# Optimization experiments

Measured on AMD Instinct MI355X. Metric: run time of the kernel, lower is better.

The kernel has to match this reference:

```python
import jax, jax.numpy as jnp
import numpy as np

DIM = 1024
HEADS = 16
HIDDEN = 2048  # dim * mlp_ratio
EPS = 1e-6


def _rmsnorm(x, scale):
    # faithful to torch: x * (scale / (norm / (sqrt(d) + eps)))
    norm = jnp.linalg.norm(x, axis=-1, keepdims=True)
    return x * (scale * (x.shape[-1] ** 0.5 + EPS) / norm)


def setup_inputs() -> dict:
    key = jax.random.key(0)
    ks = jax.random.split(key, 8)
    B, N, C = 4, 4096, DIM
    s = 0.02
    return {
        "x": jax.random.normal(ks[0], (B, N, C), dtype=jnp.float32),
        "scale1": jnp.ones((C,), jnp.float32),
        "scale2": jnp.ones((C,), jnp.float32),
        "gamma": jnp.ones((C,), jnp.float32),
        "qkv_w": jax.random.normal(ks[1], (3 * C, C), jnp.float32) * s,
        "proj_w": jax.random.normal(ks[2], (C, C), jnp.float32) * s,
        "proj_b": jnp.zeros((C,), jnp.float32),
        "conv1_w": jax.random.normal(ks[3], (HIDDEN, C), jnp.float32) * s,
        "conv1_b": jnp.zeros((HIDDEN,), jnp.float32),
        "conv2_w": jax.random.normal(ks[4], (C, HIDDEN), jnp.float32) * s,
        "conv2_b": jnp.zeros((C,), jnp.float32),
    }


def reference(x, scale1, scale2, gamma, qkv_w, proj_w, proj_b,
              conv1_w, conv1_b, conv2_w, conv2_b):
    B, N, C = x.shape
    h, d = HEADS, C // HEADS

    # ---- attention branch ----
    xn = _rmsnorm(x, scale1)
    qkv = jnp.einsum('bnc,fc->bnf', xn, qkv_w)           # [B,N,3C]
    qkv = qkv.reshape(B, N, 3, h, d).transpose(2, 0, 3, 1, 4)  # [3,B,h,N,d]
    q, k, v = qkv[0], qkv[1], qkv[2]
    phi = lambda t: jnp.exp(-0.5 * t * t)
    q, k = phi(q), phi(k)
    kv = jnp.einsum('bhnd,bhne->bhde', k, v)             # [B,h,d,d]
    z = 1.0 / (jnp.einsum('bhnd,bhd->bhn', q, k.sum(2)) + 1e-6)
    out = jnp.einsum('bhnd,bhde,bhn->bhne', q, kv, z)    # [B,h,N,d]
    out = out.transpose(0, 2, 1, 3).reshape(B, N, C)
    attn = jnp.einsum('bnc,oc->bno', out, proj_w) + proj_b
    x = x + gamma * attn

    # ---- MLP branch (1x1 convs == per-token linear) ----
    xn2 = _rmsnorm(x, scale2)
    hdd = jax.nn.gelu(jnp.einsum('bnc,hc->bnh', xn2, conv1_w) + conv1_b, approximate=False)
    mlp = jnp.einsum('bnh,ch->bnc', hdd, conv2_w) + conv2_b
    return x + gamma * mlp
```

## Files before the change

### kernel.cpp

```cpp
#include <hip/hip_runtime.h>
#include <hip/hip_bf16.h>
#include <math.h>

#define MTOK 16384

typedef __attribute__((ext_vector_type(8))) short bf16x8;
typedef __attribute__((ext_vector_type(4))) float f32x4;

__device__ __forceinline__ float bf2f(ushort u) {
  union { unsigned int u; float f; } c; c.u = ((unsigned int)u) << 16; return c.f;
}
__device__ __forceinline__ ushort f2bf(float f) {
  union { float f; unsigned int u; } c; c.f = f;
  unsigned int r = c.u + 0x7fffu + ((c.u >> 16) & 1u);
  return (ushort)(r >> 16);
}

__device__ __forceinline__ void gload_lds16(const void* g, void* l) {
  __builtin_amdgcn_global_load_lds(
      (const __attribute__((address_space(1))) unsigned int*)g,
      (__attribute__((address_space(3))) unsigned int*)l, 16, 0, 0);
}

__global__ __launch_bounds__(256)
void f32_to_bf16_k(const float* __restrict__ in, ushort* __restrict__ out, int n4) {
  int i = blockIdx.x * 256 + threadIdx.x;
  if (i >= n4) return;
  float4 v = *(const float4*)&in[(size_t)i * 4];
  ushort4 o;
  o.x = f2bf(v.x); o.y = f2bf(v.y); o.z = f2bf(v.z); o.w = f2bf(v.w);
  *(ushort4*)&out[(size_t)i * 4] = o;
}

__global__ __launch_bounds__(256)
void rmsnorm_k(const float* __restrict__ x, const float* __restrict__ scale,
               ushort* __restrict__ out) {
  __shared__ float red[4];
  int row = blockIdx.x;
  int t = threadIdx.x;
  const float* xr = x + (size_t)row * 1024;
  float4 v = *(const float4*)&xr[t * 4];
  float s = v.x*v.x + v.y*v.y + v.z*v.z + v.w*v.w;
  #pragma unroll
  for (int off = 32; off > 0; off >>= 1) s += __shfl_xor(s, off);
  if ((t & 63) == 0) red[t >> 6] = s;
  __syncthreads();
  float tot = red[0] + red[1] + red[2] + red[3];
  float rn = (32.0f + 1e-6f) / sqrtf(tot);
  float4 sc = *(const float4*)&scale[t * 4];
  ushort4 o;
  o.x = f2bf(v.x * rn * sc.x);
  o.y = f2bf(v.y * rn * sc.y);
  o.z = f2bf(v.z * rn * sc.z);
  o.w = f2bf(v.w * rn * sc.w);
  *(ushort4*)&out[(size_t)row * 1024 + t * 4] = o;
}

template<int EPI>
__global__ __launch_bounds__(256, 2)
void gemm_bt(const ushort* __restrict__ A, const ushort* __restrict__ W,
             void* __restrict__ outp, const float* __restrict__ bias,
             const float* __restrict__ gamma, const float* __restrict__ resid,
             ushort* __restrict__ kTp, ushort* __restrict__ vTp,
             int M, int F, int K) {
  __shared__ ushort lA[128 * 32];
  __shared__ ushort lB[128 * 32];
  const int tid = threadIdx.x;
  const int lane = tid & 63;
  const int w = tid >> 6;
  const int nBn = F >> 7;
  const int bm = blockIdx.x / nBn;
  const int bn = blockIdx.x % nBn;
  const int brow = bm << 7, bcol = bn << 7;
  const int wr = w >> 1, wc = w & 1;

  const int srow = (w << 4) + (lane >> 2);
  const int key = (srow >> 1) & 3;
  const int kcsrc = (lane & 3) ^ key;
  const ushort* gA0 = A + (size_t)(brow + srow) * K + kcsrc * 8;
  const ushort* gA1 = gA0 + (size_t)64 * K;
  const ushort* gB0 = W + (size_t)(bcol + srow) * K + kcsrc * 8;
  const ushort* gB1 = gB0 + (size_t)64 * K;
  ushort* lA0 = &lA[w * 512];
  ushort* lA1 = &lA[2048 + w * 512];
  ushort* lB0 = &lB[w * 512];
  ushort* lB1 = &lB[2048 + w * 512];

  const int frow = lane & 15;
  const int kq = lane >> 4;

  f32x4 acc[4][4];
  #pragma unroll
  for (int i = 0; i < 4; ++i)
    #pragma unroll
    for (int j = 0; j < 4; ++j) acc[i][j] = (f32x4){0.f, 0.f, 0.f, 0.f};

  for (int k0 = 0; k0 < K; k0 += 32) {
    gload_lds16(gA0 + k0, lA0);
    gload_lds16(gA1 + k0, lA1);
    gload_lds16(gB0 + k0, lB0);
    gload_lds16(gB1 + k0, lB1);
    __syncthreads();

    bf16x8 af[4], bfr[4];
    #pragma unroll
    for (int mi = 0; mi < 4; ++mi) {
      int row = (wr << 6) + (mi << 4) + frow;
      int off = (row << 5) + ((kq ^ ((row >> 1) & 3)) << 3);
      af[mi] = *(const bf16x8*)&lA[off];
    }
    #pragma unroll
    for (int ni = 0; ni < 4; ++ni) {
      int row = (wc << 6) + (ni << 4) + frow;
      int off = (row << 5) + ((kq ^ ((row >> 1) & 3)) << 3);
      bfr[ni] = *(const bf16x8*)&lB[off];
    }
    #pragma unroll
    for (int mi = 0; mi < 4; ++mi)
      #pragma unroll
      for (int ni = 0; ni < 4; ++ni)
        acc[mi][ni] = __builtin_amdgcn_mfma_f32_16x16x32_bf16(
            af[mi], bfr[ni], acc[mi][ni], 0, 0, 0);
    __syncthreads();
  }

  #pragma unroll
  for (int mi = 0; mi < 4; ++mi) {
    #pragma unroll
    for (int ni = 0; ni < 4; ++ni) {
      int col = bcol + (wc << 6) + (ni << 4) + frow;
      int rbase = brow + (wr << 6) + (mi << 4) + (kq << 2);
      if (EPI == 0) {
        if (col < 1024) {
          #pragma unroll
          for (int r = 0; r < 4; ++r) {
            float v = acc[mi][ni][r];
            ((ushort*)outp)[(size_t)(rbase + r) * 1024 + col] =
                f2bf(__expf(-0.5f * v * v));
          }
        } else {
          bool isk = col < 2048;
          int c = col - (isk ? 1024 : 2048);
          int b = rbase >> 12, n = rbase & 4095;
          ushort4 o;
          #pragma unroll
          for (int r = 0; r < 4; ++r) {
            float v = acc[mi][ni][r];
            if (isk) v = __expf(-0.5f * v * v);
            ((ushort*)&o)[r] = f2bf(v);
          }
          ushort* dst = (isk ? kTp : vTp) +
                        ((size_t)(b * 16 + (c >> 6)) * 64 + (c & 63)) * 4096 + n;
          *(ushort4*)dst = o;
        }
      } else {
        #pragma unroll
        for (int r = 0; r < 4; ++r) {
          int row = rbase + r;
          float v = acc[mi][ni][r];
          size_t idx = (size_t)row * F + col;
          if (EPI == 1) {
            ((float*)outp)[idx] = resid[idx] + gamma[col] * (v + bias[col]);
          } else {
            float t2 = v + bias[col];
            ((ushort*)outp)[idx] =
                f2bf(0.5f * t2 * (1.0f + erff(t2 * 0.70710678118f)));
          }
        }
      }
    }
  }
}

__global__ __launch_bounds__(256)
void attn_kv_mfma(const ushort* __restrict__ kT, const ushort* __restrict__ vT,
                  float* __restrict__ kvT, float* __restrict__ ksum) {
  __shared__ float red[4][4096];
  int bi = blockIdx.x;
  int ksl = bi & 7, h = (bi >> 3) & 15, b = bi >> 7;
  int tid = threadIdx.x, lane = tid & 63, w = tid >> 6;
  int frow = lane & 15, kq = lane >> 4;
  const size_t bh = (size_t)(b * 16 + h) * 64;
  const ushort* vb = vT + bh * 4096;
  const ushort* kb = kT + bh * 4096;
  int tk0 = ksl * 512 + w * 128;

  f32x4 acc[4][4];
  #pragma unroll
  for (int i = 0; i < 4; ++i)
    #pragma unroll
    for (int j = 0; j < 4; ++j) acc[i][j] = (f32x4){0.f, 0.f, 0.f, 0.f};
  float kpart[4] = {0.f, 0.f, 0.f, 0.f};

  #pragma unroll
  for (int kstep = 0; kstep < 4; ++kstep) {
    int tok = tk0 + kstep * 32 + kq * 8;
    bf16x8 af[4], bfr[4];
    #pragma unroll
    for (int mi = 0; mi < 4; ++mi)
      af[mi] = *(const bf16x8*)&vb[(size_t)(mi * 16 + frow) * 4096 + tok];
    #pragma unroll
    for (int ni = 0; ni < 4; ++ni) {
      bfr[ni] = *(const bf16x8*)&kb[(size_t)(ni * 16 + frow) * 4096 + tok];
      #pragma unroll
      for (int j = 0; j < 8; ++j) kpart[ni] += bf2f((ushort)bfr[ni][j]);
    }
    #pragma unroll
    for (int mi = 0; mi < 4; ++mi)
      #pragma unroll
      for (int ni = 0; ni < 4; ++ni)
        acc[mi][ni] = __builtin_amdgcn_mfma_f32_16x16x32_bf16(
            af[mi], bfr[ni], acc[mi][ni], 0, 0, 0);
  }

  #pragma unroll
  for (int ni = 0; ni < 4; ++ni) {
    kpart[ni] += __shfl_xor(kpart[ni], 16);
    kpart[ni] += __shfl_xor(kpart[ni], 32);
  }
  if (lane < 16) {
    #pragma unroll
    for (int ni = 0; ni < 4; ++ni)
      atomicAdd(&ksum[(b * 16 + h) * 64 + ni * 16 + frow], kpart[ni]);
  }

  #pragma unroll
  for (int mi = 0; mi < 4; ++mi)
    #pragma unroll
    for (int ni = 0; ni < 4; ++ni)
      #pragma unroll
      for (int r = 0; r < 4; ++r)
        red[w][(mi * 16 + kq * 4 + r) * 64 + ni * 16 + frow] = acc[mi][ni][r];
  __syncthreads();
  float* kvg = kvT + (size_t)(b * 16 + h) * 4096;
  for (int i = tid; i < 4096; i += 256) {
    float s = red[0][i] + red[1][i] + red[2][i] + red[3][i];
    atomicAdd(&kvg[i], s);
  }
}

__global__ __launch_bounds__(256)
void attn_out_mfma(const ushort* __restrict__ qb, const float* __restrict__ kvT,
                   const float* __restrict__ ksum, ushort* __restrict__ ao) {
  __shared__ ushort skv[64 * 72];
  __shared__ float sks[64];
  int bi = blockIdx.x;
  int c = bi & 15, h = (bi >> 4) & 15, b = bi >> 8;
  int tid = threadIdx.x, lane = tid & 63, w = tid >> 6;
  int frow = lane & 15, kq = lane >> 4;
  const float* kvg = kvT + (size_t)(b * 16 + h) * 4096;
  for (int i = tid; i < 4096; i += 256)
    skv[(i >> 6) * 72 + (i & 63)] = f2bf(kvg[i]);
  if (tid < 64) sks[tid] = ksum[(b * 16 + h) * 64 + tid];
  __syncthreads();

  int m0 = b * 4096 + c * 256 + w * 64;
  f32x4 acc[4][4];
  #pragma unroll
  for (int i = 0; i < 4; ++i)
    #pragma unroll
    for (int j = 0; j < 4; ++j) acc[i][j] = (f32x4){0.f, 0.f, 0.f, 0.f};
  float dp[4] = {0.f, 0.f, 0.f, 0.f};

  #pragma unroll
  for (int kst = 0; kst < 2; ++kst) {
    int d0 = kst * 32 + kq * 8;
    bf16x8 af[4], bfr[4];
    #pragma unroll
    for (int mi = 0; mi < 4; ++mi)
      af[mi] = *(const bf16x8*)&qb[(size_t)(m0 + mi * 16 + frow) * 1024 + h * 64 + d0];
    #pragma unroll
    for (int ni = 0; ni < 4; ++ni)
      bfr[ni] = *(const bf16x8*)&skv[(ni * 16 + frow) * 72 + d0];
    #pragma unroll
    for (int mi = 0; mi < 4; ++mi) {
      float s = 0.f;
      #pragma unroll
      for (int j = 0; j < 8; ++j) s += bf2f((ushort)af[mi][j]) * sks[d0 + j];
      dp[mi] += s;
    }
    #pragma unroll
    for (int mi = 0; mi < 4; ++mi)
      #pragma unroll
      for (int ni = 0; ni < 4; ++ni)
        acc[mi][ni] = __builtin_amdgcn_mfma_f32_16x16x32_bf16(
            af[mi], bfr[ni], acc[mi][ni], 0, 0, 0);
  }

  #pragma unroll
  for (int mi = 0; mi < 4; ++mi) {
    dp[mi] += __shfl_xor(dp[mi], 16);
    dp[mi] += __shfl_xor(dp[mi], 32);
  }

  #pragma unroll
  for (int mi = 0; mi < 4; ++mi)
    #pragma unroll
    for (int ni = 0; ni < 4; ++ni)
      #pragma unroll
      for (int r = 0; r < 4; ++r) {
        float dotv = __shfl(dp[mi], (kq << 2) + r);
        float z = 1.f / (dotv + 1e-6f);
        int mrow = m0 + mi * 16 + kq * 4 + r;
        ao[(size_t)mrow * 1024 + h * 64 + ni * 16 + frow] =
            f2bf(acc[mi][ni][r] * z);
      }
}

extern "C" void kernel_launch(void* const* d_in, const int* in_sizes, int n_in,
                              void* d_out, int out_size, void* d_ws, size_t ws_size,
                              hipStream_t stream) {
  const float* x       = (const float*)d_in[0];
  const float* scale1  = (const float*)d_in[1];
  const float* scale2  = (const float*)d_in[2];
  const float* gamma   = (const float*)d_in[3];
  const float* qkv_w   = (const float*)d_in[4];
  const float* proj_w  = (const float*)d_in[5];
  const float* proj_b  = (const float*)d_in[6];
  const float* conv1_w = (const float*)d_in[7];
  const float* conv1_b = (const float*)d_in[8];
  const float* conv2_w = (const float*)d_in[9];
  const float* conv2_b = (const float*)d_in[10];
  float* out = (float*)d_out;

  char* ws = (char*)d_ws;
  size_t off = 0;
  auto alloc = [&](size_t bytes) {
    void* p = ws + off;
    off += (bytes + 255) & ~(size_t)255;
    return p;
  };
  ushort* xn     = (ushort*)alloc((size_t)MTOK * 1024 * 2);
  ushort* qb     = (ushort*)alloc((size_t)MTOK * 1024 * 2);
  ushort* kT     = (ushort*)alloc((size_t)MTOK * 1024 * 2);
  ushort* vT     = (ushort*)alloc((size_t)MTOK * 1024 * 2);
  ushort* attn_o = (ushort*)alloc((size_t)MTOK * 1024 * 2);
  float*  kvT    = (float*)alloc((size_t)(4 * 16 * 64 * 64 + 4 * 16 * 64) * 4);
  float*  ksum   = kvT + 4 * 16 * 64 * 64;
  ushort* wq = (ushort*)alloc((size_t)3072 * 1024 * 2);
  ushort* wp = (ushort*)alloc((size_t)1024 * 1024 * 2);
  ushort* w1 = (ushort*)alloc((size_t)2048 * 1024 * 2);
  ushort* w2 = (ushort*)alloc((size_t)1024 * 2048 * 2);
  ushort* hid = kT;
  if (off > ws_size) return;

  hipMemsetAsync(kvT, 0, (size_t)(4 * 16 * 64 * 64 + 4 * 16 * 64) * 4, stream);
  f32_to_bf16_k<<<3072, 256, 0, stream>>>(qkv_w, wq, 786432);
  f32_to_bf16_k<<<1024, 256, 0, stream>>>(proj_w, wp, 262144);
  f32_to_bf16_k<<<2048, 256, 0, stream>>>(conv1_w, w1, 524288);
  f32_to_bf16_k<<<2048, 256, 0, stream>>>(conv2_w, w2, 524288);

  rmsnorm_k<<<MTOK, 256, 0, stream>>>(x, scale1, xn);
  gemm_bt<0><<<128 * 24, 256, 0, stream>>>(xn, wq, qb, nullptr, nullptr, nullptr,
                                           kT, vT, MTOK, 3072, 1024);
  attn_kv_mfma<<<512, 256, 0, stream>>>(kT, vT, kvT, ksum);
  attn_out_mfma<<<1024, 256, 0, stream>>>(qb, kvT, ksum, attn_o);
  gemm_bt<1><<<128 * 8, 256, 0, stream>>>(attn_o, wp, out, proj_b, gamma, x,
                                          nullptr, nullptr, MTOK, 1024, 1024);

  rmsnorm_k<<<MTOK, 256, 0, stream>>>(out, scale2, xn);
  gemm_bt<2><<<128 * 16, 256, 0, stream>>>(xn, w1, hid, conv1_b, nullptr, nullptr,
                                           nullptr, nullptr, MTOK, 2048, 1024);
  gemm_bt<1><<<128 * 8, 256, 0, stream>>>(hid, w2, out, conv2_b, gamma, out,
                                          nullptr, nullptr, MTOK, 1024, 2048);
}
```

Baseline: 503.6 us.

## Replace 128x128 GEMM with 256x256 double-buffered 8-wave GEMM with swizzled grid

```diff
diff --git a/kernel.cpp b/kernel.cpp
--- a/kernel.cpp
+++ b/kernel.cpp
@@ -57,79 +57,147 @@
 }
 
 template<int EPI>
-__global__ __launch_bounds__(256, 2)
-void gemm_bt(const ushort* __restrict__ A, const ushort* __restrict__ W,
+__global__ __launch_bounds__(512, 2)
+void gemm256(const ushort* __restrict__ A, const ushort* __restrict__ W,
              void* __restrict__ outp, const float* __restrict__ bias,
              const float* __restrict__ gamma, const float* __restrict__ resid,
              ushort* __restrict__ kTp, ushort* __restrict__ vTp,
-             int M, int F, int K) {
-  __shared__ ushort lA[128 * 32];
-  __shared__ ushort lB[128 * 32];
+             int nBn, int K) {
+  __shared__ ushort lds[65536];
   const int tid = threadIdx.x;
   const int lane = tid & 63;
   const int w = tid >> 6;
-  const int nBn = F >> 7;
-  const int bm = blockIdx.x / nBn;
-  const int bn = blockIdx.x % nBn;
-  const int brow = bm << 7, bcol = bn << 7;
-  const int wr = w >> 1, wc = w & 1;
-
-  const int srow = (w << 4) + (lane >> 2);
-  const int key = (srow >> 1) & 3;
-  const int kcsrc = (lane & 3) ^ key;
-  const ushort* gA0 = A + (size_t)(brow + srow) * K + kcsrc * 8;
-  const ushort* gA1 = gA0 + (size_t)64 * K;
-  const ushort* gB0 = W + (size_t)(bcol + srow) * K + kcsrc * 8;
-  const ushort* gB1 = gB0 + (size_t)64 * K;
-  ushort* lA0 = &lA[w * 512];
-  ushort* lA1 = &lA[2048 + w * 512];
-  ushort* lB0 = &lB[w * 512];
-  ushort* lB1 = &lB[2048 + w * 512];
-
-  const int frow = lane & 15;
-  const int kq = lane >> 4;
-
-  f32x4 acc[4][4];
-  #pragma unroll
-  for (int i = 0; i < 4; ++i)
+  const int wm = w >> 2, wn = w & 3;
+  const int frow = lane & 15, kq = lane >> 4;
+  const int F = nBn << 8;
+
+  const int swz = ((int)blockIdx.x & 7) * ((int)gridDim.x >> 3) + ((int)blockIdx.x >> 3);
+  const int bm = swz / nBn, bn = swz % nBn;
+  const int brow = bm << 8, bcol = bn << 8;
+
+  const int srow = (w << 4) + frow;
+  const ushort* pa = A + (size_t)(brow + srow) * K + (kq << 3);
+  const ushort* pb = W + (size_t)(bcol + srow) * K + (kq << 3);
+  const int sdA = w << 10;
+  const int sdB = 16384 + (w << 10);
+  const int ra = (wm << 13) + (lane << 3);
+  const int rb = 16384 + ((wn >> 1) << 13) + ((wn & 1) << 12) + (lane << 3);
+
+  auto stA = [&](int b, int h, int k0) {
+    const ushort* s = pa + (size_t)(h << 7) * K + k0;
+    ushort* d = &lds[(b << 15) + (h << 13) + sdA];
+    gload_lds16(s, d);
+    gload_lds16(s + 32, d + 512);
+  };
+  auto stB = [&](int b, int h, int k0) {
+    const ushort* s = pb + (size_t)(h << 7) * K + k0;
+    ushort* d = &lds[(b << 15) + (h << 13) + sdB];
+    gload_lds16(s, d);
+    gload_lds16(s + 32, d + 512);
+  };
+
+  const int NT = K >> 6;
+  stA(0, 0, 0); stA(0, 1, 0);
+  stB(0, 0, 0); stB(0, 1, 0);
+  stA(1, 0, 64); stA(1, 1, 64);
+  asm volatile("s_waitcnt vmcnt(4)\ns_barrier" ::: "memory");
+
+  f32x4 acc[8][4];
+  #pragma unroll
+  for (int i = 0; i < 8; ++i)
     #pragma unroll
     for (int j = 0; j < 4; ++j) acc[i][j] = (f32x4){0.f, 0.f, 0.f, 0.f};
 
-  for (int k0 = 0; k0 < K; k0 += 32) {
-    gload_lds16(gA0 + k0, lA0);
-    gload_lds16(gA1 + k0, lA1);
-    gload_lds16(gB0 + k0, lB0);
-    gload_lds16(gB1 + k0, lB1);
-    __syncthreads();
-
-    bf16x8 af[4], bfr[4];
-    #pragma unroll
-    for (int mi = 0; mi < 4; ++mi) {
-      int row = (wr << 6) + (mi << 4) + frow;
-      int off = (row << 5) + ((kq ^ ((row >> 1) & 3)) << 3);
-      af[mi] = *(const bf16x8*)&lA[off];
-    }
+  for (int t = 0; t < NT; ++t) {
+    const int b = t & 1, bb = b << 15;
+    bf16x8 ar[4][2], br[2][2];
+
+    if (t + 1 < NT) stB(b ^ 1, 0, (t + 1) << 6);
+    #pragma unroll
+    for (int mi = 0; mi < 4; ++mi)
+      #pragma unroll
+      for (int ks = 0; ks < 2; ++ks)
+        ar[mi][ks] = *(const bf16x8*)&lds[bb + ra + (mi << 10) + (ks << 9)];
+    #pragma unroll
+    for (int ni = 0; ni < 2; ++ni)
+      #pragma unroll
+      for (int ks = 0; ks < 2; ++ks)
+        br[ni][ks] = *(const bf16x8*)&lds[bb + rb + (ni << 10) + (ks << 9)];
+    __builtin_amdgcn_s_setprio(1);
+    #pragma unroll
+    for (int mi = 0; mi < 4; ++mi)
+      #pragma unroll
+      for (int ni = 0; ni < 2; ++ni)
+        #pragma unroll
+        for (int ks = 0; ks < 2; ++ks)
+          acc[mi][ni] = __builtin_amdgcn_mfma_f32_16x16x32_bf16(
+              ar[mi][ks], br[ni][ks], acc[mi][ni], 0, 0, 0);
+    __builtin_amdgcn_s_setprio(0);
+
+    if (t + 1 < NT) stB(b ^ 1, 1, (t + 1) << 6);
+    #pragma unroll
+    for (int ni = 0; ni < 2; ++ni)
+      #pragma unroll
+      for (int ks = 0; ks < 2; ++ks)
+        br[ni][ks] = *(const bf16x8*)&lds[bb + rb + ((2 + ni) << 10) + (ks << 9)];
+    __builtin_amdgcn_s_setprio(1);
+    #pragma unroll
+    for (int mi = 0; mi < 4; ++mi)
+      #pragma unroll
+      for (int ni = 0; ni < 2; ++ni)
+        #pragma unroll
+        for (int ks = 0; ks < 2; ++ks)
+          acc[mi][2 + ni] = __builtin_amdgcn_mfma_f32_16x16x32_bf16(
+              ar[mi][ks], br[ni][ks], acc[mi][2 + ni], 0, 0, 0);
+    __builtin_amdgcn_s_setprio(0);
+
+    #pragma unroll
+    for (int mi = 0; mi < 4; ++mi)
+      #pragma unroll
+      for (int ks = 0; ks < 2; ++ks)
+        ar[mi][ks] = *(const bf16x8*)&lds[bb + ra + ((4 + mi) << 10) + (ks << 9)];
+    __builtin_amdgcn_s_setprio(1);
+    #pragma unroll
+    for (int mi = 0; mi < 4; ++mi)
+      #pragma unroll
+      for (int ni = 0; ni < 2; ++ni)
+        #pragma unroll
+        for (int ks = 0; ks < 2; ++ks)
+          acc[4 + mi][2 + ni] = __builtin_amdgcn_mfma_f32_16x16x32_bf16(
+              ar[mi][ks], br[ni][ks], acc[4 + mi][2 + ni], 0, 0, 0);
+    __builtin_amdgcn_s_setprio(0);
+
+    asm volatile("s_waitcnt lgkmcnt(0)\ns_barrier" ::: "memory");
+
+    if (t + 2 < NT) { stA(b, 0, (t + 2) << 6); stA(b, 1, (t + 2) << 6); }
+    #pragma unroll
+    for (int ni = 0; ni < 2; ++ni)
+      #pragma unroll
+      for (int ks = 0; ks < 2; ++ks)
+        br[ni][ks] = *(const bf16x8*)&lds[bb + rb + (ni << 10) + (ks << 9)];
+    __builtin_amdgcn_s_setprio(1);
+    #pragma unroll
+    for (int mi = 0; mi < 4; ++mi)
+      #pragma unroll
+      for (int ni = 0; ni < 2; ++ni)
+        #pragma unroll
+        for (int ks = 0; ks < 2; ++ks)
+          acc[4 + mi][ni] = __builtin_amdgcn_mfma_f32_16x16x32_bf16(
+              ar[mi][ks], br[ni][ks], acc[4 + mi][ni], 0, 0, 0);
+    __builtin_amdgcn_s_setprio(0);
+
+    if (t + 2 < NT)
+      asm volatile("s_waitcnt lgkmcnt(0) vmcnt(4)\ns_barrier" ::: "memory");
+    else
+      asm volatile("s_waitcnt lgkmcnt(0) vmcnt(0)\ns_barrier" ::: "memory");
+  }
+
+  #pragma unroll
+  for (int mi = 0; mi < 8; ++mi) {
     #pragma unroll
     for (int ni = 0; ni < 4; ++ni) {
-      int row = (wc << 6) + (ni << 4) + frow;
-      int off = (row << 5) + ((kq ^ ((row >> 1) & 3)) << 3);
-      bfr[ni] = *(const bf16x8*)&lB[off];
-    }
-    #pragma unroll
-    for (int mi = 0; mi < 4; ++mi)
-      #pragma unroll
-      for (int ni = 0; ni < 4; ++ni)
-        acc[mi][ni] = __builtin_amdgcn_mfma_f32_16x16x32_bf16(
-            af[mi], bfr[ni], acc[mi][ni], 0, 0, 0);
-    __syncthreads();
-  }
-
-  #pragma unroll
-  for (int mi = 0; mi < 4; ++mi) {
-    #pragma unroll
-    for (int ni = 0; ni < 4; ++ni) {
-      int col = bcol + (wc << 6) + (ni << 4) + frow;
-      int rbase = brow + (wr << 6) + (mi << 4) + (kq << 2);
+      int col = bcol + (wn << 6) + (ni << 4) + frow;
+      int rbase = brow + (wm << 7) + (mi << 4) + (kq << 2);
       if (EPI == 0) {
         if (col < 1024) {
           #pragma unroll
@@ -351,16 +419,16 @@
   f32_to_bf16_k<<<2048, 256, 0, stream>>>(conv2_w, w2, 524288);
 
   rmsnorm_k<<<MTOK, 256, 0, stream>>>(x, scale1, xn);
-  gemm_bt<0><<<128 * 24, 256, 0, stream>>>(xn, wq, qb, nullptr, nullptr, nullptr,
-                                           kT, vT, MTOK, 3072, 1024);
+  gemm256<0><<<768, 512, 0, stream>>>(xn, wq, qb, nullptr, nullptr, nullptr,
+                                      kT, vT, 12, 1024);
   attn_kv_mfma<<<512, 256, 0, stream>>>(kT, vT, kvT, ksum);
   attn_out_mfma<<<1024, 256, 0, stream>>>(qb, kvT, ksum, attn_o);
-  gemm_bt<1><<<128 * 8, 256, 0, stream>>>(attn_o, wp, out, proj_b, gamma, x,
-                                          nullptr, nullptr, MTOK, 1024, 1024);
+  gemm256<1><<<256, 512, 0, stream>>>(attn_o, wp, out, proj_b, gamma, x,
+                                      nullptr, nullptr, 4, 1024);
 
   rmsnorm_k<<<MTOK, 256, 0, stream>>>(out, scale2, xn);
-  gemm_bt<2><<<128 * 16, 256, 0, stream>>>(xn, w1, hid, conv1_b, nullptr, nullptr,
-                                           nullptr, nullptr, MTOK, 2048, 1024);
-  gemm_bt<1><<<128 * 8, 256, 0, stream>>>(hid, w2, out, conv2_b, gamma, out,
-                                          nullptr, nullptr, MTOK, 1024, 2048);
-}
+  gemm256<2><<<512, 512, 0, stream>>>(xn, w1, hid, conv1_b, nullptr, nullptr,
+                                      nullptr, nullptr, 8, 1024);
+  gemm256<1><<<256, 512, 0, stream>>>(hid, w2, out, conv2_b, gamma, out,
+                                      nullptr, nullptr, 4, 2048);
+}
```

New measurement: 584.0 us. +16.0%, slower.
